# Performance work log

Hardware: AMD Instinct MI355X
Metric: run time of the kernel (lower is better)

## Reference

```python
import jax, jax.numpy as jnp
import numpy as np
import math

B = 8192
LAT, COND, OUT = 64, 256, 512
HID, E, NLAYER, GH = 1024, 8, 3, 128
INPUT = LAT + COND          # 320
INTER = LAT + HID           # 1088
EPS = 1e-5


def _ln(x):
    # F.layer_norm(input, input.shape[1:]) -> no affine, eps=1e-5, over last dim
    m = jnp.mean(x, axis=-1, keepdims=True)
    v = jnp.var(x, axis=-1, keepdims=True)
    return (x - m) * jax.lax.rsqrt(v + EPS)


def setup_inputs() -> dict:
    key = jax.random.key(0)
    ks = jax.random.split(key, 24)
    d = {}
    d['z'] = jax.random.normal(ks[0], (B, LAT), jnp.float32)
    d['c'] = jax.random.normal(ks[1], (B, COND), jnp.float32)
    # gate MLP params (PyTorch Linear default init scale ~ 1/sqrt(fan_in))
    gate_dims = [(INPUT, GH), (GH, GH), (GH, E)]
    for i, (fi, fo) in enumerate(gate_dims):
        s = 1.0 / math.sqrt(fi)
        d[f'g{i}_w'] = jax.random.uniform(ks[2 + 2 * i], (fi, fo), jnp.float32, -s, s)
        d[f'g{i}_b'] = jax.random.uniform(ks[3 + 2 * i], (fo,), jnp.float32, -s, s)
    # expert decoder layers: weight [E, in, out], bias [E, out], stdv = 1/sqrt(in)
    for i in range(NLAYER + 1):
        fi = INPUT if i == 0 else INTER
        fo = HID if i != NLAYER else OUT
        s = 1.0 / math.sqrt(fi)
        d[f'w{i}'] = jax.random.uniform(ks[8 + 2 * i], (E, fi, fo), jnp.float32, -s, s)
        d[f'b{i}'] = jax.random.uniform(ks[9 + 2 * i], (E, fo), jnp.float32, -s, s)
    return d


def reference(z, c, g0_w, g0_b, g1_w, g1_b, g2_w, g2_b,
              w0, b0, w1, b1, w2, b2, w3, b3):
    x = jnp.concatenate([z, c], axis=-1)                    # [B, INPUT]
    h = jax.nn.elu(x @ g0_w + g0_b)
    h = jax.nn.elu(h @ g1_w + g1_b)
    coeff = jax.nn.softmax(h @ g2_w + g2_b, axis=-1)        # [B, E]

    layer_out = c
    layers = [(w0, b0, True), (w1, b1, True), (w2, b2, True), (w3, b3, False)]
    for w, b, act in layers:
        inp = _ln(jnp.concatenate([z, layer_out], axis=-1))  # [B, J]
        per = jnp.einsum('bj,ejk->ebk', inp, w)              # per-expert outputs
        out = jnp.einsum('be,ebk->bk', coeff, per) + coeff @ b
        layer_out = jax.nn.elu(out) if act else out
    return layer_out
```

## Files before the change

### kernel.cpp

```cpp
#include <hip/hip_runtime.h>
#include <cstdint>
#include <cstddef>

#define B_ROWS 8192
#define E_EXP  8

typedef unsigned short ushort_t;
typedef short bf16x8 __attribute__((ext_vector_type(8)));
typedef float f32x4  __attribute__((ext_vector_type(4)));

__device__ __forceinline__ ushort_t f2b(float f) {
  union { float f; unsigned int i; } v; v.f = f;
  unsigned int u = v.i;
  unsigned int r = (u + 0x7fffu + ((u >> 16) & 1u)) >> 16;
  return (ushort_t)r;
}
__device__ __forceinline__ float eluf(float x) {
  return x > 0.f ? x : (__expf(x) - 1.f);
}

__global__ void transpose_k(const float* __restrict__ src,
                            ushort_t* __restrict__ dst, int R, int C) {
  __shared__ ushort_t tile[64][65];
  int c0 = blockIdx.x * 64, r0 = blockIdx.y * 64;
  int x = threadIdx.x, y = threadIdx.y;
#pragma unroll
  for (int i = 0; i < 4; ++i)
    tile[y + 16 * i][x] = f2b(src[(size_t)(r0 + y + 16 * i) * C + c0 + x]);
  __syncthreads();
#pragma unroll
  for (int i = 0; i < 4; ++i)
    dst[(size_t)(c0 + y + 16 * i) * R + r0 + x] = tile[x][y + 16 * i];
}

__global__ __launch_bounds__(128) void gate_k(
    const float* __restrict__ z, const float* __restrict__ c,
    const float* __restrict__ g0w, const float* __restrict__ g0b,
    const float* __restrict__ g1w, const float* __restrict__ g1b,
    const float* __restrict__ g2w, const float* __restrict__ g2b,
    float* __restrict__ coeff, float* __restrict__ rat2,
    float* __restrict__ rat4) {
  __shared__ float xs[4][320];
  __shared__ float h1[4][128];
  __shared__ float h2[4][128];
  __shared__ float lg[4][8];
  __shared__ float pr[4][8];
  int t = threadIdx.x;
  int r0 = blockIdx.x * 4;
  for (int idx = t; idx < 4 * 320; idx += 128) {
    int r = idx / 320, j = idx % 320;
    xs[r][j] = (j < 64) ? z[(size_t)(r0 + r) * 64 + j]
                        : c[(size_t)(r0 + r) * 256 + j - 64];
  }
  __syncthreads();
  {
    float bb = g0b[t];
    float a0 = bb, a1 = bb, a2 = bb, a3 = bb;
    for (int j = 0; j < 320; ++j) {
      float wv = g0w[j * 128 + t];
      a0 += xs[0][j] * wv; a1 += xs[1][j] * wv;
      a2 += xs[2][j] * wv; a3 += xs[3][j] * wv;
    }
    h1[0][t] = eluf(a0); h1[1][t] = eluf(a1);
    h1[2][t] = eluf(a2); h1[3][t] = eluf(a3);
  }
  __syncthreads();
  {
    float bb = g1b[t];
    float a0 = bb, a1 = bb, a2 = bb, a3 = bb;
    for (int j = 0; j < 128; ++j) {
      float wv = g1w[j * 128 + t];
      a0 += h1[0][j] * wv; a1 += h1[1][j] * wv;
      a2 += h1[2][j] * wv; a3 += h1[3][j] * wv;
    }
    h2[0][t] = eluf(a0); h2[1][t] = eluf(a1);
    h2[2][t] = eluf(a2); h2[3][t] = eluf(a3);
  }
  __syncthreads();
  if (t < 32) {
    int r = t >> 3, e = t & 7;
    float a = g2b[e];
    for (int j = 0; j < 128; ++j) a += h2[r][j] * g2w[j * 8 + e];
    lg[r][e] = a;
  }
  __syncthreads();
  if (t < 32) {
    int r = t >> 3, e = t & 7;
    float mx = lg[r][0];
#pragma unroll
    for (int i = 1; i < 8; ++i) mx = fmaxf(mx, lg[r][i]);
    float s = 0.f;
#pragma unroll
    for (int i = 0; i < 8; ++i) s += __expf(lg[r][i] - mx);
    float p = __expf(lg[r][e] - mx) / s;
    coeff[(size_t)(r0 + r) * 8 + e] = p;
    pr[r][e] = p;
  }
  __syncthreads();
  if (t < 32) {
    int r = t >> 3, e = t & 7;
    float pe = pr[r][e];
    float ratio = (e < 7) ? pe / fmaxf(pr[r][e + 1], 1e-30f) : pe;
    rat2[(size_t)(r0 + r) * 8 + e] = (e == 3 || e == 7) ? pe : ratio;
    rat4[(size_t)(r0 + r) * 8 + e] = (e & 1) ? pe : ratio;
  }
}

__global__ __launch_bounds__(128) void ln_concat_k(
    const float* __restrict__ z, const float* __restrict__ p0,
    const float* __restrict__ p1, const float* __restrict__ cf,
    const float* __restrict__ bias, ushort_t* __restrict__ out,
    int Pw, int J) {
  int row = blockIdx.x, t = threadIdx.x;
  float vals[9];
  int n = (J + 127) >> 7;
  float cr[8];
  if (p1) {
#pragma unroll
    for (int e = 0; e < 8; ++e) cr[e] = cf[(size_t)row * 8 + e];
  }
  float s = 0.f, s2 = 0.f;
  for (int k = 0; k < n; ++k) {
    int i = t + (k << 7);
    float x = 0.f;
    if (i < J) {
      if (i < 64) {
        x = z[(size_t)row * 64 + i];
      } else if (p1) {
        int j = i - 64;
        float v = p0[(size_t)row * Pw + j] + p1[(size_t)row * Pw + j];
#pragma unroll
        for (int e = 0; e < 8; ++e) v += cr[e] * bias[(size_t)e * Pw + j];
        x = eluf(v);
      } else {
        x = p0[(size_t)row * Pw + i - 64];
      }
    }
    vals[k] = x; s += x; s2 += x * x;
  }
  for (int off = 32; off > 0; off >>= 1) {
    s += __shfl_down(s, off);
    s2 += __shfl_down(s2, off);
  }
  __shared__ float red[4];
  int wid = t >> 6, lane = t & 63;
  if (lane == 0) { red[wid * 2] = s; red[wid * 2 + 1] = s2; }
  __syncthreads();
  float S = red[0] + red[2], S2 = red[1] + red[3];
  float inv = 1.f / (float)J;
  float m = S * inv;
  float var = S2 * inv - m * m;
  float rstd = rsqrtf(var + 1e-5f);
  for (int k = 0; k < n; ++k) {
    int i = t + (k << 7);
    if (i < J) out[(size_t)row * J + i] = f2b((vals[k] - m) * rstd);
  }
}

__device__ __forceinline__ void gload16(const void* g, void* l) {
  __builtin_amdgcn_global_load_lds(
      (const __attribute__((address_space(1))) void*)g,
      (__attribute__((address_space(3))) void*)l, 16, 0, 0);
}

#define LOAD_B(Wb)                                                         \
  _Pragma("unroll") for (int fn = 0; fn < 4; ++fn) bf[fn] =                \
      *(const bf16x8*)((Wb) + (wn * 4 + fn) * 512 + l * 8);

#define QUAD(Ab, MB)                                                       \
  {                                                                        \
    bf16x8 af[4];                                                          \
    _Pragma("unroll") for (int q = 0; q < 4; ++q) af[q] =                  \
        *(const bf16x8*)((Ab) + (wm * 8 + (MB) + q) * 512 + l * 8);        \
    __builtin_amdgcn_s_setprio(1);                                         \
    _Pragma("unroll") for (int q = 0; q < 4; ++q)                          \
        _Pragma("unroll") for (int fn = 0; fn < 4; ++fn) acc[(MB) + q][fn] = \
            __builtin_amdgcn_mfma_f32_16x16x32_bf16(af[q], bf[fn],         \
                                                    acc[(MB) + q][fn], 0, 0, 0); \
    __builtin_amdgcn_s_setprio(0);                                         \
  }

__global__ __launch_bounds__(512, 2) void moe_gemm_k(
    const ushort_t* __restrict__ inp,
    const ushort_t* __restrict__ wT,
    const float* __restrict__ scales,
    float* __restrict__ outp,
    int J, int K, int ne) {
  const int Kd = E_EXP * J;
  const int nj = J >> 6;
  const int nt = ne * nj;
  __shared__ short As[2][2][16 * 512];
  __shared__ short Wsm[2][2][16 * 512];
  __shared__ float scale_s[256 * 9];

  const int t = threadIdx.x;
  const int w = t >> 6, l = t & 63;
  const int wm = w >> 2, wn = w & 3;
  const int bt = blockIdx.x, ct = blockIdx.y, ez = blockIdx.z;
  const int e0 = ez * ne;
  outp += (size_t)ez * (size_t)B_ROWS * (size_t)K;

#pragma unroll
  for (int i = 0; i < 4; ++i) {
    int idx = t + (i << 9);
    int rw = idx >> 3, e = idx & 7;
    scale_s[rw * 9 + e] = scales[(size_t)(bt * 256 + rw) * 8 + e];
  }

  size_t abase[2], wbase[2];
#pragma unroll
  for (int i = 0; i < 2; ++i) {
    int g = w * 2 + i;
    abase[i] = (size_t)(bt * 256 + g * 16 + (l & 15)) * J + ((l >> 4) * 8);
    wbase[i] = (size_t)(ct * 256 + g * 16 + (l & 15)) * Kd + (size_t)e0 * J +
               ((l >> 4) * 8);
  }
  int s_acol = 0, s_wcol = 0, sjt = 0;

  auto stageA = [&](int nb, int ks) {
    short* d = &As[nb][ks][w * 2 * 512];
    gload16(inp + abase[0] + s_acol + ks * 32, d);
    gload16(inp + abase[1] + s_acol + ks * 32, d + 512);
  };
  auto stageW = [&](int nb, int ks) {
    short* d = &Wsm[nb][ks][w * 2 * 512];
    gload16(wT + wbase[0] + s_wcol + ks * 32, d);
    gload16(wT + wbase[1] + s_wcol + ks * 32, d + 512);
  };
  auto advance = [&]() {
    s_wcol += 64;
    if (++sjt == nj) { sjt = 0; s_acol = 0; } else { s_acol += 64; }
  };

  f32x4 acc[8][4];
#pragma unroll
  for (int fm = 0; fm < 8; ++fm)
#pragma unroll
    for (int fn = 0; fn < 4; ++fn) acc[fm][fn] = (f32x4){0.f, 0.f, 0.f, 0.f};

  stageA(0, 0); stageW(0, 0); stageA(0, 1); stageW(0, 1); advance();
  __syncthreads();

  int cjt = 0, cle = 0;
  for (int tp = 0; tp < nt; ++tp) {
    const int b = tp & 1, nb = b ^ 1;
    const bool more = (tp + 1 < nt);
    const short* Ab0 = &As[b][0][0];
    const short* Ab1 = &As[b][1][0];
    const short* Wb0 = &Wsm[b][0][0];
    const short* Wb1 = &Wsm[b][1][0];
    bf16x8 bf[4];

    if (more) stageA(nb, 0);
    LOAD_B(Wb0);
    QUAD(Ab0, 0);
    if (more) stageW(nb, 0);
    QUAD(Ab0, 4);
    if (more) asm volatile("s_waitcnt vmcnt(4)" ::: "memory");
    else      asm volatile("s_waitcnt vmcnt(0)" ::: "memory");
    asm volatile("s_barrier" ::: "memory");
    if (more) stageA(nb, 1);
    LOAD_B(Wb1);
    QUAD(Ab1, 0);
    if (more) { stageW(nb, 1); advance(); }
    QUAD(Ab1, 4);
    if (++cjt == nj) {
      cjt = 0;
      int e = e0 + cle;
      ++cle;
#pragma unroll
      for (int fi = 0; fi < 8; ++fi) {
        int rbase = wm * 128 + fi * 16 + ((l >> 4) << 2);
#pragma unroll
        for (int rr = 0; rr < 4; ++rr) {
          float rv = scale_s[(rbase + rr) * 9 + e];
#pragma unroll
          for (int fn = 0; fn < 4; ++fn) acc[fi][fn][rr] *= rv;
        }
      }
    }
    if (more) asm volatile("s_waitcnt vmcnt(4)" ::: "memory");
    else      asm volatile("s_waitcnt vmcnt(0)" ::: "memory");
    asm volatile("s_barrier" ::: "memory");
  }

#pragma unroll
  for (int fi = 0; fi < 8; ++fi) {
#pragma unroll
    for (int rr = 0; rr < 4; ++rr) {
      int row = wm * 128 + fi * 16 + ((l >> 4) << 2) + rr;
      size_t orow = (size_t)(bt * 256 + row) * K + ct * 256;
#pragma unroll
      for (int fn = 0; fn < 4; ++fn) {
        int col = wn * 64 + fn * 16 + (l & 15);
        outp[orow + col] = acc[fi][fn][rr];
      }
    }
  }
}

__global__ __launch_bounds__(256) void combine4_k(
    const float* __restrict__ pb, const float* __restrict__ cf,
    const float* __restrict__ bias, float* __restrict__ out, int K) {
  size_t i4 = (size_t)blockIdx.x * 256 + threadIdx.x;
  size_t total = (size_t)B_ROWS * (size_t)K;
  size_t base = i4 * 4;
  if (base >= total) return;
  int row = (int)(base / (size_t)K);
  int col = (int)(base % (size_t)K);
  size_t s4 = total >> 2;
  const f32x4* p4 = (const f32x4*)pb;
  f32x4 v = p4[i4] + p4[i4 + s4] + p4[i4 + 2 * s4] + p4[i4 + 3 * s4];
#pragma unroll
  for (int e = 0; e < 8; ++e) {
    float ce = cf[(size_t)row * 8 + e];
    f32x4 bv = *(const f32x4*)(bias + (size_t)e * K + col);
    v += ce * bv;
  }
  ((f32x4*)out)[i4] = v;
}

extern "C" void kernel_launch(void* const* d_in, const int* in_sizes, int n_in,
                              void* d_out, int out_size, void* d_ws, size_t ws_size,
                              hipStream_t stream) {
  const float* z   = (const float*)d_in[0];
  const float* c   = (const float*)d_in[1];
  const float* g0w = (const float*)d_in[2];
  const float* g0b = (const float*)d_in[3];
  const float* g1w = (const float*)d_in[4];
  const float* g1b = (const float*)d_in[5];
  const float* g2w = (const float*)d_in[6];
  const float* g2b = (const float*)d_in[7];
  const float* w0  = (const float*)d_in[8];
  const float* b0  = (const float*)d_in[9];
  const float* w1  = (const float*)d_in[10];
  const float* b1  = (const float*)d_in[11];
  const float* w2  = (const float*)d_in[12];
  const float* b2  = (const float*)d_in[13];
  const float* w3  = (const float*)d_in[14];
  const float* b3  = (const float*)d_in[15];

  char* ws = (char*)d_ws;
  size_t o = 0;
  auto alloc = [&](size_t bytes) {
    void* p = ws + o;
    o += (bytes + 255) & ~(size_t)255;
    return p;
  };
  ushort_t* wT0 = (ushort_t*)alloc((size_t)2560 * 1024 * 2);
  ushort_t* wT1 = (ushort_t*)alloc((size_t)8704 * 1024 * 2);
  ushort_t* wT2 = (ushort_t*)alloc((size_t)8704 * 1024 * 2);
  ushort_t* wT3 = (ushort_t*)alloc((size_t)8704 * 512 * 2);
  float*    cf   = (float*)alloc((size_t)B_ROWS * 8 * 4);
  float*    rat2 = (float*)alloc((size_t)B_ROWS * 8 * 4);
  float*    rat4 = (float*)alloc((size_t)B_ROWS * 8 * 4);
  ushort_t* inp  = (ushort_t*)alloc((size_t)B_ROWS * 1088 * 2);
  float*    pb   = (float*)alloc((size_t)2 * B_ROWS * 1024 * 4);

  dim3 tb(64, 16);
  transpose_k<<<dim3(1024 / 64, 2560 / 64), tb, 0, stream>>>(w0, wT0, 2560, 1024);
  transpose_k<<<dim3(1024 / 64, 8704 / 64), tb, 0, stream>>>(w1, wT1, 8704, 1024);
  transpose_k<<<dim3(1024 / 64, 8704 / 64), tb, 0, stream>>>(w2, wT2, 8704, 1024);
  transpose_k<<<dim3(512 / 64, 8704 / 64), tb, 0, stream>>>(w3, wT3, 8704, 512);

  gate_k<<<B_ROWS / 4, 128, 0, stream>>>(z, c, g0w, g0b, g1w, g1b, g2w, g2b,
                                         cf, rat2, rat4);

  float* p1v = pb + (size_t)B_ROWS * 1024;

  ln_concat_k<<<B_ROWS, 128, 0, stream>>>(z, c, nullptr, nullptr, nullptr,
                                          inp, 256, 320);
  moe_gemm_k<<<dim3(32, 4, 2), 512, 0, stream>>>(inp, wT0, rat2, pb, 320, 1024, 4);
  ln_concat_k<<<B_ROWS, 128, 0, stream>>>(z, pb, p1v, cf, b0, inp, 1024, 1088);
  moe_gemm_k<<<dim3(32, 4, 2), 512, 0, stream>>>(inp, wT1, rat2, pb, 1088, 1024, 4);
  ln_concat_k<<<B_ROWS, 128, 0, stream>>>(z, pb, p1v, cf, b1, inp, 1024, 1088);
  moe_gemm_k<<<dim3(32, 4, 2), 512, 0, stream>>>(inp, wT2, rat2, pb, 1088, 1024, 4);
  ln_concat_k<<<B_ROWS, 128, 0, stream>>>(z, pb, p1v, cf, b2, inp, 1024, 1088);
  moe_gemm_k<<<dim3(32, 2, 4), 512, 0, stream>>>(inp, wT3, rat4, pb, 1088, 512, 2);
  combine4_k<<<(B_ROWS * 512) / 1024, 256, 0, stream>>>(pb, cf, b3,
                                                        (float*)d_out, 512);
}
```

Before: 712.5 us.

## Split MoE GEMM loop into barrier-separated load and MFMA phases

Restructures the main tile loop of the expert GEMM so that each half-tile first issues its LDS fragment reads and the next global-to-LDS stage, then hits a workgroup barrier and a scheduling fence before running its block of MFMAs. Two sched barriers per phase keep the compiler from interleaving memory and matrix instructions, aiming for a cleaner ping-pong between waves in memory and waves in MFMA. The cost is many more s_barrier instructions per tile, and warps are forced into lockstep. The last iteration now waits with vmcnt(4) instead of vmcnt(0), which relaxes the drain of outstanding loads and could leave in-flight data unsynchronised.

Measured after the change: 700.5 us. Within noise of the previous version (-1.7%).

```diff
diff --git a/kernel.cpp b/kernel.cpp
--- a/kernel.cpp
+++ b/kernel.cpp
@@ -163,22 +163,25 @@
       (__attribute__((address_space(3))) void*)l, 16, 0, 0);
 }
 
-#define LOAD_B(Wb)                                                         \
+#define BAR() asm volatile("s_barrier" ::: "memory")
+#define VMC4() asm volatile("s_waitcnt vmcnt(4)" ::: "memory")
+#define FENCE() __builtin_amdgcn_sched_barrier(0)
+
+#define LOADB(Wb)                                                          \
   _Pragma("unroll") for (int fn = 0; fn < 4; ++fn) bf[fn] =                \
       *(const bf16x8*)((Wb) + (wn * 4 + fn) * 512 + l * 8);
 
-#define QUAD(Ab, MB)                                                       \
-  {                                                                        \
-    bf16x8 af[4];                                                          \
-    _Pragma("unroll") for (int q = 0; q < 4; ++q) af[q] =                  \
-        *(const bf16x8*)((Ab) + (wm * 8 + (MB) + q) * 512 + l * 8);        \
-    __builtin_amdgcn_s_setprio(1);                                         \
-    _Pragma("unroll") for (int q = 0; q < 4; ++q)                          \
-        _Pragma("unroll") for (int fn = 0; fn < 4; ++fn) acc[(MB) + q][fn] = \
-            __builtin_amdgcn_mfma_f32_16x16x32_bf16(af[q], bf[fn],         \
-                                                    acc[(MB) + q][fn], 0, 0, 0); \
-    __builtin_amdgcn_s_setprio(0);                                         \
-  }
+#define LOADA(Ab, MB)                                                      \
+  _Pragma("unroll") for (int q = 0; q < 4; ++q) af[q] =                    \
+      *(const bf16x8*)((Ab) + (wm * 8 + (MB) + q) * 512 + l * 8);
+
+#define DOMFMA(MB)                                                         \
+  __builtin_amdgcn_s_setprio(1);                                           \
+  _Pragma("unroll") for (int q = 0; q < 4; ++q)                            \
+      _Pragma("unroll") for (int fn = 0; fn < 4; ++fn) acc[(MB) + q][fn] = \
+          __builtin_amdgcn_mfma_f32_16x16x32_bf16(af[q], bf[fn],           \
+                                                  acc[(MB) + q][fn], 0, 0, 0); \
+  __builtin_amdgcn_s_setprio(0);
 
 __global__ __launch_bounds__(512, 2) void moe_gemm_k(
     const ushort_t* __restrict__ inp,
@@ -245,25 +248,38 @@
   for (int tp = 0; tp < nt; ++tp) {
     const int b = tp & 1, nb = b ^ 1;
     const bool more = (tp + 1 < nt);
-    const short* Ab0 = &As[b][0][0];
-    const short* Ab1 = &As[b][1][0];
-    const short* Wb0 = &Wsm[b][0][0];
-    const short* Wb1 = &Wsm[b][1][0];
-    bf16x8 bf[4];
-
+    const short* A0 = &As[b][0][0];
+    const short* A1 = &As[b][1][0];
+    const short* W0 = &Wsm[b][0][0];
+    const short* W1 = &Wsm[b][1][0];
+    bf16x8 bf[4], af[4];
+
+    LOADB(W0);
+    LOADA(A0, 0);
     if (more) stageA(nb, 0);
-    LOAD_B(Wb0);
-    QUAD(Ab0, 0);
+    BAR(); FENCE();
+    DOMFMA(0);
+    FENCE();
+    BAR();
+    LOADA(A0, 4);
     if (more) stageW(nb, 0);
-    QUAD(Ab0, 4);
-    if (more) asm volatile("s_waitcnt vmcnt(4)" ::: "memory");
-    else      asm volatile("s_waitcnt vmcnt(0)" ::: "memory");
-    asm volatile("s_barrier" ::: "memory");
+    BAR(); FENCE();
+    DOMFMA(4);
+    FENCE();
+    VMC4();
+    BAR();
+    LOADB(W1);
+    LOADA(A1, 0);
     if (more) stageA(nb, 1);
-    LOAD_B(Wb1);
-    QUAD(Ab1, 0);
+    BAR(); FENCE();
+    DOMFMA(0);
+    FENCE();
+    BAR();
+    LOADA(A1, 4);
     if (more) { stageW(nb, 1); advance(); }
-    QUAD(Ab1, 4);
+    BAR(); FENCE();
+    DOMFMA(4);
+    FENCE();
     if (++cjt == nj) {
       cjt = 0;
       int e = e0 + cle;
@@ -279,9 +295,8 @@
         }
       }
     }
-    if (more) asm volatile("s_waitcnt vmcnt(4)" ::: "memory");
-    else      asm volatile("s_waitcnt vmcnt(0)" ::: "memory");
-    asm volatile("s_barrier" ::: "memory");
+    VMC4();
+    BAR();
   }
 
 #pragma unroll
```

## Software-pipeline LDS fragment reads across MFMA groups and issue all stages at once

Applied to the files above, without the earlier changes.

Restructures the MoE GEMM main loop so that all global-to-LDS loads for the next tile are issued at the start of the iteration, rather than interleaved in two halves. It also double-buffers register fragments so that LDS reads for the next MFMA group overlap the current MFMA group. The first fragments of the next tile are preloaded after the barrier. This drops one barrier per iteration and hides LDS read latency, at the cost of more VGPRs, which may hurt occupancy at 2 blocks per CU. It also waits on vmcnt(0) at every iteration.

Measured after the change: 763.6 us. 7.2% more time.

```diff
diff --git a/kernel.cpp b/kernel.cpp
--- a/kernel.cpp
+++ b/kernel.cpp
@@ -163,22 +163,21 @@
       (__attribute__((address_space(3))) void*)l, 16, 0, 0);
 }
 
-#define LOAD_B(Wb)                                                         \
-  _Pragma("unroll") for (int fn = 0; fn < 4; ++fn) bf[fn] =                \
+#define RD_B(dst, Wb)                                                      \
+  _Pragma("unroll") for (int fn = 0; fn < 4; ++fn) dst[fn] =               \
       *(const bf16x8*)((Wb) + (wn * 4 + fn) * 512 + l * 8);
 
-#define QUAD(Ab, MB)                                                       \
-  {                                                                        \
-    bf16x8 af[4];                                                          \
-    _Pragma("unroll") for (int q = 0; q < 4; ++q) af[q] =                  \
-        *(const bf16x8*)((Ab) + (wm * 8 + (MB) + q) * 512 + l * 8);        \
-    __builtin_amdgcn_s_setprio(1);                                         \
-    _Pragma("unroll") for (int q = 0; q < 4; ++q)                          \
-        _Pragma("unroll") for (int fn = 0; fn < 4; ++fn) acc[(MB) + q][fn] = \
-            __builtin_amdgcn_mfma_f32_16x16x32_bf16(af[q], bf[fn],         \
-                                                    acc[(MB) + q][fn], 0, 0, 0); \
-    __builtin_amdgcn_s_setprio(0);                                         \
-  }
+#define RD_A(dst, Ab, MB)                                                  \
+  _Pragma("unroll") for (int q = 0; q < 4; ++q) dst[q] =                   \
+      *(const bf16x8*)((Ab) + (wm * 8 + (MB) + q) * 512 + l * 8);
+
+#define MM(MB, AA, BB)                                                     \
+  __builtin_amdgcn_s_setprio(1);                                           \
+  _Pragma("unroll") for (int q = 0; q < 4; ++q)                            \
+      _Pragma("unroll") for (int fn = 0; fn < 4; ++fn) acc[(MB) + q][fn] = \
+          __builtin_amdgcn_mfma_f32_16x16x32_bf16(AA[q], BB[fn],           \
+                                                  acc[(MB) + q][fn], 0, 0, 0); \
+  __builtin_amdgcn_s_setprio(0);
 
 __global__ __launch_bounds__(512, 2) void moe_gemm_k(
     const ushort_t* __restrict__ inp,
@@ -217,17 +216,16 @@
   }
   int s_acol = 0, s_wcol = 0, sjt = 0;
 
-  auto stageA = [&](int nb, int ks) {
-    short* d = &As[nb][ks][w * 2 * 512];
-    gload16(inp + abase[0] + s_acol + ks * 32, d);
-    gload16(inp + abase[1] + s_acol + ks * 32, d + 512);
-  };
-  auto stageW = [&](int nb, int ks) {
-    short* d = &Wsm[nb][ks][w * 2 * 512];
-    gload16(wT + wbase[0] + s_wcol + ks * 32, d);
-    gload16(wT + wbase[1] + s_wcol + ks * 32, d + 512);
-  };
-  auto advance = [&]() {
+  auto stageAll = [&](int nb) {
+#pragma unroll
+    for (int ks = 0; ks < 2; ++ks) {
+      short* dA = &As[nb][ks][w * 2 * 512];
+      gload16(inp + abase[0] + s_acol + ks * 32, dA);
+      gload16(inp + abase[1] + s_acol + ks * 32, dA + 512);
+      short* dW = &Wsm[nb][ks][w * 2 * 512];
+      gload16(wT + wbase[0] + s_wcol + ks * 32, dW);
+      gload16(wT + wbase[1] + s_wcol + ks * 32, dW + 512);
+    }
     s_wcol += 64;
     if (++sjt == nj) { sjt = 0; s_acol = 0; } else { s_acol += 64; }
   };
@@ -238,32 +236,32 @@
 #pragma unroll
     for (int fn = 0; fn < 4; ++fn) acc[fm][fn] = (f32x4){0.f, 0.f, 0.f, 0.f};
 
-  stageA(0, 0); stageW(0, 0); stageA(0, 1); stageW(0, 1); advance();
-  __syncthreads();
+  bf16x8 fb0[4], fb1[4], fa0[4], fa1[4];
+
+  stageAll(0);
+  __syncthreads();
+  RD_B(fb0, &Wsm[0][0][0]);
+  RD_A(fa0, &As[0][0][0], 0);
 
   int cjt = 0, cle = 0;
   for (int tp = 0; tp < nt; ++tp) {
     const int b = tp & 1, nb = b ^ 1;
     const bool more = (tp + 1 < nt);
-    const short* Ab0 = &As[b][0][0];
-    const short* Ab1 = &As[b][1][0];
-    const short* Wb0 = &Wsm[b][0][0];
-    const short* Wb1 = &Wsm[b][1][0];
-    bf16x8 bf[4];
-
-    if (more) stageA(nb, 0);
-    LOAD_B(Wb0);
-    QUAD(Ab0, 0);
-    if (more) stageW(nb, 0);
-    QUAD(Ab0, 4);
-    if (more) asm volatile("s_waitcnt vmcnt(4)" ::: "memory");
-    else      asm volatile("s_waitcnt vmcnt(0)" ::: "memory");
-    asm volatile("s_barrier" ::: "memory");
-    if (more) stageA(nb, 1);
-    LOAD_B(Wb1);
-    QUAD(Ab1, 0);
-    if (more) { stageW(nb, 1); advance(); }
-    QUAD(Ab1, 4);
+    const short* A0 = &As[b][0][0];
+    const short* A1 = &As[b][1][0];
+    const short* W1 = &Wsm[b][1][0];
+
+    if (more) stageAll(nb);
+
+    RD_A(fa1, A0, 4);
+    MM(0, fa0, fb0);
+    RD_B(fb1, W1);
+    RD_A(fa0, A1, 0);
+    MM(4, fa1, fb0);
+    RD_A(fa1, A1, 4);
+    MM(0, fa0, fb1);
+    MM(4, fa1, fb1);
+
     if (++cjt == nj) {
       cjt = 0;
       int e = e0 + cle;
@@ -279,9 +277,13 @@
         }
       }
     }
-    if (more) asm volatile("s_waitcnt vmcnt(4)" ::: "memory");
-    else      asm volatile("s_waitcnt vmcnt(0)" ::: "memory");
+
+    asm volatile("s_waitcnt vmcnt(0)" ::: "memory");
     asm volatile("s_barrier" ::: "memory");
+    if (more) {
+      RD_B(fb0, &Wsm[nb][0][0]);
+      RD_A(fa0, &As[nb][0][0], 0);
+    }
   }
 
 #pragma unroll
```

## Switch MoE GEMM to 32x32x16 MFMA tiles and unroll gate MLP loops

Applied to the files above, without the earlier changes.

Replaces the 16x16x32 bf16 MFMA tiling in the expert GEMM with 32x32x16 MFMA instructions. Each wave now holds a 4x2 grid of 32x32 accumulators, and the LDS fragment reads, the per-expert row scaling and the output store indexing are remapped to the new accumulator layout. The larger MFMA shape is meant to cut the number of LDS fragment reads and instruction issues per unit of math. The gate MLP inner loops are also unrolled by four, with float4 reads from shared memory. The new fragment layout risks LDS bank conflicts and changes register pressure.

New measurement: 740.6 us. 3.9% more time.

```diff
diff --git a/kernel.cpp b/kernel.cpp
--- a/kernel.cpp
+++ b/kernel.cpp
@@ -8,6 +8,7 @@
 typedef unsigned short ushort_t;
 typedef short bf16x8 __attribute__((ext_vector_type(8)));
 typedef float f32x4  __attribute__((ext_vector_type(4)));
+typedef float f32x16 __attribute__((ext_vector_type(16)));
 
 __device__ __forceinline__ ushort_t f2b(float f) {
   union { float f; unsigned int i; } v; v.f = f;
@@ -56,10 +57,19 @@
   {
     float bb = g0b[t];
     float a0 = bb, a1 = bb, a2 = bb, a3 = bb;
-    for (int j = 0; j < 320; ++j) {
-      float wv = g0w[j * 128 + t];
-      a0 += xs[0][j] * wv; a1 += xs[1][j] * wv;
-      a2 += xs[2][j] * wv; a3 += xs[3][j] * wv;
+    for (int j = 0; j < 320; j += 4) {
+      float w0 = g0w[j * 128 + t];
+      float w1 = g0w[(j + 1) * 128 + t];
+      float w2 = g0w[(j + 2) * 128 + t];
+      float w3 = g0w[(j + 3) * 128 + t];
+      float4 x0 = *(const float4*)&xs[0][j];
+      float4 x1 = *(const float4*)&xs[1][j];
+      float4 x2 = *(const float4*)&xs[2][j];
+      float4 x3 = *(const float4*)&xs[3][j];
+      a0 += x0.x * w0 + x0.y * w1 + x0.z * w2 + x0.w * w3;
+      a1 += x1.x * w0 + x1.y * w1 + x1.z * w2 + x1.w * w3;
+      a2 += x2.x * w0 + x2.y * w1 + x2.z * w2 + x2.w * w3;
+      a3 += x3.x * w0 + x3.y * w1 + x3.z * w2 + x3.w * w3;
     }
     h1[0][t] = eluf(a0); h1[1][t] = eluf(a1);
     h1[2][t] = eluf(a2); h1[3][t] = eluf(a3);
@@ -68,10 +78,19 @@
   {
     float bb = g1b[t];
     float a0 = bb, a1 = bb, a2 = bb, a3 = bb;
-    for (int j = 0; j < 128; ++j) {
-      float wv = g1w[j * 128 + t];
-      a0 += h1[0][j] * wv; a1 += h1[1][j] * wv;
-      a2 += h1[2][j] * wv; a3 += h1[3][j] * wv;
+    for (int j = 0; j < 128; j += 4) {
+      float w0 = g1w[j * 128 + t];
+      float w1 = g1w[(j + 1) * 128 + t];
+      float w2 = g1w[(j + 2) * 128 + t];
+      float w3 = g1w[(j + 3) * 128 + t];
+      float4 x0 = *(const float4*)&h1[0][j];
+      float4 x1 = *(const float4*)&h1[1][j];
+      float4 x2 = *(const float4*)&h1[2][j];
+      float4 x3 = *(const float4*)&h1[3][j];
+      a0 += x0.x * w0 + x0.y * w1 + x0.z * w2 + x0.w * w3;
+      a1 += x1.x * w0 + x1.y * w1 + x1.z * w2 + x1.w * w3;
+      a2 += x2.x * w0 + x2.y * w1 + x2.z * w2 + x2.w * w3;
+      a3 += x3.x * w0 + x3.y * w1 + x3.z * w2 + x3.w * w3;
     }
     h2[0][t] = eluf(a0); h2[1][t] = eluf(a1);
     h2[2][t] = eluf(a2); h2[3][t] = eluf(a3);
@@ -162,23 +181,6 @@
       (const __attribute__((address_space(1))) void*)g,
       (__attribute__((address_space(3))) void*)l, 16, 0, 0);
 }
-
-#define LOAD_B(Wb)                                                         \
-  _Pragma("unroll") for (int fn = 0; fn < 4; ++fn) bf[fn] =                \
-      *(const bf16x8*)((Wb) + (wn * 4 + fn) * 512 + l * 8);
-
-#define QUAD(Ab, MB)                                                       \
-  {                                                                        \
-    bf16x8 af[4];                                                          \
-    _Pragma("unroll") for (int q = 0; q < 4; ++q) af[q] =                  \
-        *(const bf16x8*)((Ab) + (wm * 8 + (MB) + q) * 512 + l * 8);        \
-    __builtin_amdgcn_s_setprio(1);                                         \
-    _Pragma("unroll") for (int q = 0; q < 4; ++q)                          \
-        _Pragma("unroll") for (int fn = 0; fn < 4; ++fn) acc[(MB) + q][fn] = \
-            __builtin_amdgcn_mfma_f32_16x16x32_bf16(af[q], bf[fn],         \
-                                                    acc[(MB) + q][fn], 0, 0, 0); \
-    __builtin_amdgcn_s_setprio(0);                                         \
-  }
 
 __global__ __launch_bounds__(512, 2) void moe_gemm_k(
     const ushort_t* __restrict__ inp,
@@ -196,6 +198,10 @@
   const int t = threadIdx.x;
   const int w = t >> 6, l = t & 63;
   const int wm = w >> 2, wn = w & 3;
+  const int lr  = l & 31;
+  const int lh  = (l & 31) >> 4;
+  const int lk  = l >> 5;
+  const int lro = (l & 15) * 8;
   const int bt = blockIdx.x, ct = blockIdx.y, ez = blockIdx.z;
   const int e0 = ez * ne;
   outp += (size_t)ez * (size_t)B_ROWS * (size_t)K;
@@ -232,11 +238,36 @@
     if (++sjt == nj) { sjt = 0; s_acol = 0; } else { s_acol += 64; }
   };
 
-  f32x4 acc[8][4];
-#pragma unroll
-  for (int fm = 0; fm < 8; ++fm)
-#pragma unroll
-    for (int fn = 0; fn < 4; ++fn) acc[fm][fn] = (f32x4){0.f, 0.f, 0.f, 0.f};
+  f32x16 acc[4][2];
+#pragma unroll
+  for (int R = 0; R < 4; ++R)
+#pragma unroll
+    for (int C = 0; C < 2; ++C)
+#pragma unroll
+      for (int q = 0; q < 16; ++q) acc[R][C][q] = 0.f;
+
+  auto rdA = [&](bf16x8* dst, const short* half, int s) {
+#pragma unroll
+    for (int R = 0; R < 4; ++R)
+      dst[R] = *(const bf16x8*)(half + (wm * 8 + R * 2 + lh) * 512 + lro +
+                                (s * 2 + lk) * 128);
+  };
+  auto rdW = [&](bf16x8(*dst)[2], const short* half) {
+#pragma unroll
+    for (int s = 0; s < 2; ++s)
+#pragma unroll
+      for (int C = 0; C < 2; ++C)
+        dst[s][C] = *(const bf16x8*)(half + (wn * 4 + C * 2 + lh) * 512 + lro +
+                                     (s * 2 + lk) * 128);
+  };
+
+#define MM8(AF, BF)                                                        \
+  __builtin_amdgcn_s_setprio(1);                                           \
+  _Pragma("unroll") for (int R = 0; R < 4; ++R)                            \
+      _Pragma("unroll") for (int C = 0; C < 2; ++C) acc[R][C] =            \
+          __builtin_amdgcn_mfma_f32_32x32x16_bf16(AF[R], BF[C],            \
+                                                  acc[R][C], 0, 0, 0);     \
+  __builtin_amdgcn_s_setprio(0);
 
   stageA(0, 0); stageW(0, 0); stageA(0, 1); stageW(0, 1); advance();
   __syncthreads();
@@ -245,37 +276,41 @@
   for (int tp = 0; tp < nt; ++tp) {
     const int b = tp & 1, nb = b ^ 1;
     const bool more = (tp + 1 < nt);
-    const short* Ab0 = &As[b][0][0];
-    const short* Ab1 = &As[b][1][0];
-    const short* Wb0 = &Wsm[b][0][0];
-    const short* Wb1 = &Wsm[b][1][0];
-    bf16x8 bf[4];
+    const short* A0 = &As[b][0][0];
+    const short* A1 = &As[b][1][0];
+    const short* W0 = &Wsm[b][0][0];
+    const short* W1 = &Wsm[b][1][0];
+    bf16x8 af[4], bf[2][2];
 
     if (more) stageA(nb, 0);
-    LOAD_B(Wb0);
-    QUAD(Ab0, 0);
+    rdW(bf, W0);
+    rdA(af, A0, 0);
+    MM8(af, bf[0]);
     if (more) stageW(nb, 0);
-    QUAD(Ab0, 4);
+    rdA(af, A0, 1);
+    MM8(af, bf[1]);
     if (more) asm volatile("s_waitcnt vmcnt(4)" ::: "memory");
     else      asm volatile("s_waitcnt vmcnt(0)" ::: "memory");
     asm volatile("s_barrier" ::: "memory");
     if (more) stageA(nb, 1);
-    LOAD_B(Wb1);
-    QUAD(Ab1, 0);
+    rdW(bf, W1);
+    rdA(af, A1, 0);
+    MM8(af, bf[0]);
     if (more) { stageW(nb, 1); advance(); }
-    QUAD(Ab1, 4);
+    rdA(af, A1, 1);
+    MM8(af, bf[1]);
     if (++cjt == nj) {
       cjt = 0;
       int e = e0 + cle;
       ++cle;
 #pragma unroll
-      for (int fi = 0; fi < 8; ++fi) {
-        int rbase = wm * 128 + fi * 16 + ((l >> 4) << 2);
-#pragma unroll
-        for (int rr = 0; rr < 4; ++rr) {
-          float rv = scale_s[(rbase + rr) * 9 + e];
-#pragma unroll
-          for (int fn = 0; fn < 4; ++fn) acc[fi][fn][rr] *= rv;
+      for (int R = 0; R < 4; ++R) {
+#pragma unroll
+        for (int q = 0; q < 16; ++q) {
+          int row = wm * 128 + R * 32 + (q & 3) + 8 * (q >> 2) + 4 * lk;
+          float rv = scale_s[row * 9 + e];
+          acc[R][0][q] *= rv;
+          acc[R][1][q] *= rv;
         }
       }
     }
@@ -285,16 +320,14 @@
   }
 
 #pragma unroll
-  for (int fi = 0; fi < 8; ++fi) {
-#pragma unroll
-    for (int rr = 0; rr < 4; ++rr) {
-      int row = wm * 128 + fi * 16 + ((l >> 4) << 2) + rr;
+  for (int R = 0; R < 4; ++R) {
+#pragma unroll
+    for (int q = 0; q < 16; ++q) {
+      int row = wm * 128 + R * 32 + (q & 3) + 8 * (q >> 2) + 4 * lk;
       size_t orow = (size_t)(bt * 256 + row) * K + ct * 256;
 #pragma unroll
-      for (int fn = 0; fn < 4; ++fn) {
-        int col = wn * 64 + fn * 16 + (l & 15);
-        outp[orow + col] = acc[fi][fn][rr];
-      }
+      for (int C = 0; C < 2; ++C)
+        outp[orow + wn * 64 + C * 32 + lr] = acc[R][C][q];
     }
   }
 }
```
